# Optimization experiments

Hardware: AMD Instinct MI355X
Metric: run time of the kernel (lower is better)

## Reference

```python
import jax, jax.numpy as jnp
import numpy as np
import math

B, L, H, D = 4, 2048, 8, 64
FACTOR = 5
SAMPLE_K = min(FACTOR * int(np.ceil(np.log(L))), L)  # U_part = 40
N_TOP = min(FACTOR * int(np.ceil(np.log(L))), L)     # u = 40


def setup_inputs() -> dict:
    key = jax.random.key(0)
    kq, kk, kv, ki = jax.random.split(key, 4)
    queries = jax.random.normal(kq, (B, L, H, D), dtype=jnp.float32)
    keys = jax.random.normal(kk, (B, L, H, D), dtype=jnp.float32)
    values = jax.random.normal(kv, (B, L, H, D), dtype=jnp.float32)
    # ProbSparse random key sampling indices (torch.randint(L_K, (L_Q, sample_k)))
    index_sample = jax.random.randint(ki, (L, SAMPLE_K), 0, L, dtype=jnp.int64)
    return {"queries": queries, "keys": keys, "values": values,
            "index_sample": index_sample}


def reference(queries, keys, values, index_sample):
    # [B, L, H, D] -> [B, H, L, D]
    Q = jnp.transpose(queries, (0, 2, 1, 3))
    K = jnp.transpose(keys, (0, 2, 1, 3))
    V = jnp.transpose(values, (0, 2, 1, 3))
    L_K = K.shape[2]

    # --- _prob_QK ---
    # gather sampled keys per query: [B, H, L_Q, sample_k, D]
    K_sample = K[:, :, index_sample, :]
    # sampled QK dots: [B, H, L_Q, sample_k]
    Q_K_sample = jnp.einsum('bhld,bhlsd->bhls', Q, K_sample)
    # sparsity measurement M = max - mean
    M = Q_K_sample.max(axis=-1) - Q_K_sample.sum(axis=-1) / L_K  # [B, H, L_Q]
    _, M_top = jax.lax.top_k(M, N_TOP)  # [B, H, n_top]
    # gather top queries: [B, H, n_top, D]
    Q_reduce = jnp.take_along_axis(Q, M_top[..., None], axis=2)
    # reduced scores against all keys: [B, H, n_top, L_K]
    scores_top = jnp.einsum('bhud,bhkd->bhuk', Q_reduce, K)

    # --- forward tail ---
    scale = 1.0 / math.sqrt(D)
    attn = jax.nn.softmax(scores_top * scale, axis=-1)  # dropout = identity (eval)
    context = jnp.einsum('bhuk,bhkd->bhud', attn, V)  # [B, H, n_top, D]
    # [B, n_top, H, D]
    return jnp.transpose(context, (0, 2, 1, 3))
```

## Files before the change

### kernel.cpp

```cpp
#include <hip/hip_runtime.h>
#include <hip/hip_bf16.h>

#define BB 4
#define LL 2048
#define HH 8
#define DD 64
#define SK 40
#define NT 40
#define CH 256
#define NCH (LL / CH)
#define QH 20

#define WS 10
#define HB 68
#define RS (HH * HB)

__global__ __launch_bounds__(256) void compute_m_kernel(
        const float* __restrict__ Q, const float* __restrict__ K,
        const int* __restrict__ idx, float* __restrict__ M) {
    __shared__ float kbuf[4][2][2 * RS];
    __shared__ int sidx[SK];
    __shared__ float2 mlpart[4][HH];

    int blk = blockIdx.x;
    int x = blk & 7, g = blk >> 3;
    int b = x >> 1;
    int l = (g << 1) | (x & 1);
    int t = threadIdx.x;

    if (t < SK) sidx[t] = idx[(size_t)l * SK + t];

    int lane = t & 63, w = t >> 6;
    int s_lo = lane >> 5;
    int h    = (lane >> 2) & 7;
    int q    = lane & 3;

    const float4* Qb = (const float4*)(Q + ((size_t)b * LL + l) * 512 + h * 64 + q * 16);
    float4 qf0 = Qb[0], qf1 = Qb[1], qf2 = Qb[2], qf3 = Qb[3];

    const float* Kb = K + (size_t)b * LL * 512;

    int r  = lane >> 5;
    int cw = lane & 31;
    int av = cw >> 4;
    int c4 = (4 * cw) & 63;
    __syncthreads();

    float4 ra0, ra1, ra2, ra3;
    float4 rb0, rb1, rb2, rb3;

    #define LOADX(p, d0, d1, d2, d3) do {                                       \
        const float* src = Kb + (size_t)sidx[w * WS + (p) * 2 + r] * 512        \
                         + cw * 4;                                              \
        d0 = *(const float4*)(src);                                             \
        d1 = *(const float4*)(src + 128);                                       \
        d2 = *(const float4*)(src + 256);                                       \
        d3 = *(const float4*)(src + 384);                                       \
    } while (0)
    #define WRITEX(slot, d0, d1, d2, d3) do {                                   \
        float* base = &kbuf[w][slot][r * RS + c4];                              \
        *(float4*)(base + (av + 0) * HB) = d0;                                  \
        *(float4*)(base + (av + 2) * HB) = d1;                                  \
        *(float4*)(base + (av + 4) * HB) = d2;                                  \
        *(float4*)(base + (av + 6) * HB) = d3;                                  \
    } while (0)
    #define CONSUME(slot) do {                                                  \
        asm volatile("s_waitcnt lgkmcnt(0)" ::: "memory");                      \
        const float* kb = &kbuf[w][slot][s_lo * RS + h * HB + q * 16];          \
        float4 k0 = *(const float4*)(kb);                                       \
        float4 k1 = *(const float4*)(kb + 4);                                   \
        float4 k2 = *(const float4*)(kb + 8);                                   \
        float4 k3 = *(const float4*)(kb + 12);                                  \
        float pd = qf0.x*k0.x + qf0.y*k0.y + qf0.z*k0.z + qf0.w*k0.w            \
                 + qf1.x*k1.x + qf1.y*k1.y + qf1.z*k1.z + qf1.w*k1.w            \
                 + qf2.x*k2.x + qf2.y*k2.y + qf2.z*k2.z + qf2.w*k2.w            \
                 + qf3.x*k3.x + qf3.y*k3.y + qf3.z*k3.z + qf3.w*k3.w;           \
        pd += __shfl_xor(pd, 1, 64);                                            \
        pd += __shfl_xor(pd, 2, 64);                                            \
        mx = fmaxf(mx, pd);                                                     \
        sm += pd;                                                               \
    } while (0)

    float mx = -INFINITY, sm = 0.0f;

    LOADX(0, ra0, ra1, ra2, ra3);
    LOADX(1, rb0, rb1, rb2, rb3);
    WRITEX(0, ra0, ra1, ra2, ra3);

    LOADX(2, ra0, ra1, ra2, ra3);
    CONSUME(0);
    WRITEX(1, rb0, rb1, rb2, rb3);

    LOADX(3, rb0, rb1, rb2, rb3);
    CONSUME(1);
    WRITEX(0, ra0, ra1, ra2, ra3);

    LOADX(4, ra0, ra1, ra2, ra3);
    CONSUME(0);
    WRITEX(1, rb0, rb1, rb2, rb3);

    CONSUME(1);
    WRITEX(0, ra0, ra1, ra2, ra3);

    CONSUME(0);

    #undef LOADX
    #undef WRITEX
    #undef CONSUME

    mx = fmaxf(mx, __shfl_xor(mx, 32, 64));
    sm += __shfl_xor(sm, 32, 64);

    if ((lane & 0x23) == 0)
        mlpart[w][h] = make_float2(mx, sm);
    __syncthreads();

    if (t < HH) {
        float MX = -INFINITY, SM = 0.0f;
        #pragma unroll
        for (int w2 = 0; w2 < 4; ++w2) {
            float2 ml = mlpart[w2][t];
            MX = fmaxf(MX, ml.x);
            SM += ml.y;
        }
        M[((size_t)b * HH + t) * LL + l] = MX - SM * (1.0f / (float)LL);
    }
}

__global__ __launch_bounds__(256) void topk_kernel(const float* __restrict__ M,
                                                   int* __restrict__ topi) {
    __shared__ unsigned long long keys[LL];
    __shared__ unsigned long long wmax[4];
    __shared__ int win;
    int bh = blockIdx.x;
    int t  = threadIdx.x;
    int lane = t & 63, w = t >> 6;

    unsigned long long kmax = 0ULL;
    #pragma unroll
    for (int j = 0; j < 8; ++j) {
        int i = t + 256 * j;
        unsigned int bits = __float_as_uint(M[(size_t)bh * LL + i]);
        bits = (bits & 0x80000000u) ? ~bits : (bits | 0x80000000u);
        unsigned long long k = ((unsigned long long)bits << 11)
                             | (unsigned int)(LL - 1 - i);
        keys[i] = k;
        if (k > kmax) kmax = k;
    }
    __syncthreads();

    for (int u = 0; u < NT; ++u) {
        unsigned long long k = kmax;
        #pragma unroll
        for (int off = 32; off >= 1; off >>= 1) {
            unsigned long long o = __shfl_xor(k, off, 64);
            if (o > k) k = o;
        }
        if (lane == 0) wmax[w] = k;
        __syncthreads();
        if (t == 0) {
            unsigned long long k0 = wmax[0];
            if (wmax[1] > k0) k0 = wmax[1];
            if (wmax[2] > k0) k0 = wmax[2];
            if (wmax[3] > k0) k0 = wmax[3];
            int i = (LL - 1) - (int)(k0 & 0x7FF);
            topi[bh * NT + u] = i;
            keys[i] = 0ULL;
            win = i;
        }
        __syncthreads();
        if ((win & 255) == t) {
            kmax = 0ULL;
            #pragma unroll
            for (int j = 0; j < 8; ++j) {
                unsigned long long kk = keys[t + 256 * j];
                if (kk > kmax) kmax = kk;
            }
        }
    }
}

__global__ __launch_bounds__(256, 3) void attn_kernel(
        const float* __restrict__ Q, const float* __restrict__ K,
        const float* __restrict__ V, const int* __restrict__ topi,
        float2* __restrict__ pml, float* __restrict__ po) {
    __shared__ float  qs[QH][DD];
    __shared__ float4 e4buf[4][64];
    __shared__ float  oarea[4][QH][DD];
    __shared__ float  mlarea[4][QH][2];

    int blk = blockIdx.x;
    int qh  = blk >> 8;
    int cc2 = blk & 255;
    int c   = cc2 & (NCH - 1);
    int bh  = cc2 >> 3;
    int h = bh & (HH - 1), b = bh >> 3;
    int t = threadIdx.x, lane = t & 63, w = t >> 6;
    int u0 = qh * QH;

    for (int i = t; i < QH * DD; i += 256) {
        int u = i >> 6, d = i & 63;
        int lq = topi[bh * NT + u0 + u];
        qs[u][d] = Q[(((size_t)b * LL + lq) * HH + h) * DD + d];
    }

    int key = c * CH + w * 64 + lane;
    const float4* kr = (const float4*)&K[(((size_t)b * LL + key) * HH + h) * DD];
    float4 kreg[16];
    #pragma unroll
    for (int j = 0; j < 16; ++j) kreg[j] = kr[j];

    float vcol[64];
    const float* vb = &V[(((size_t)b * LL + c * CH + w * 64) * HH + h) * DD + lane];
    #pragma unroll
    for (int j = 0; j < 64; ++j) vcol[j] = vb[(size_t)j * HH * DD];

    __syncthreads();

    for (int uq = 0; uq < QH / 4; ++uq) {
        float o0 = 0, o1 = 0, o2 = 0, o3 = 0;
        float mv0, mv1, mv2, mv3, lv0, lv1, lv2, lv3;
        float4 ev;
        #pragma unroll
        for (int j = 0; j < 4; ++j) {
            int u = uq * 4 + j;
            const float4* q4 = (const float4*)&qs[u][0];
            float s = 0.0f;
            #pragma unroll
            for (int cc = 0; cc < 16; ++cc) {
                float4 qv = q4[cc];
                s += qv.x * kreg[cc].x + qv.y * kreg[cc].y
                   + qv.z * kreg[cc].z + qv.w * kreg[cc].w;
            }
            s *= 0.125f;
            float m = s;
            #pragma unroll
            for (int off = 32; off >= 1; off >>= 1)
                m = fmaxf(m, __shfl_xor(m, off, 64));
            float e = __expf(s - m);
            float ls = e;
            #pragma unroll
            for (int off = 32; off >= 1; off >>= 1)
                ls += __shfl_xor(ls, off, 64);
            if (j == 0) { mv0 = m; lv0 = ls; ev.x = e; }
            if (j == 1) { mv1 = m; lv1 = ls; ev.y = e; }
            if (j == 2) { mv2 = m; lv2 = ls; ev.z = e; }
            if (j == 3) { mv3 = m; lv3 = ls; ev.w = e; }
        }
        e4buf[w][lane] = ev;
        asm volatile("s_waitcnt lgkmcnt(0)" ::: "memory");
        #pragma unroll
        for (int l2 = 0; l2 < 64; ++l2) {
            float4 e = e4buf[w][l2];
            float  v = vcol[l2];
            o0 += e.x * v; o1 += e.y * v; o2 += e.z * v; o3 += e.w * v;
        }
        oarea[w][uq * 4 + 0][lane] = o0;
        oarea[w][uq * 4 + 1][lane] = o1;
        oarea[w][uq * 4 + 2][lane] = o2;
        oarea[w][uq * 4 + 3][lane] = o3;
        if (lane == 0) {
            mlarea[w][uq * 4 + 0][0] = mv0; mlarea[w][uq * 4 + 0][1] = lv0;
            mlarea[w][uq * 4 + 1][0] = mv1; mlarea[w][uq * 4 + 1][1] = lv1;
            mlarea[w][uq * 4 + 2][0] = mv2; mlarea[w][uq * 4 + 2][1] = lv2;
            mlarea[w][uq * 4 + 3][0] = mv3; mlarea[w][uq * 4 + 3][1] = lv3;
        }
    }
    __syncthreads();

    for (int i = t; i < QH * DD; i += 256) {
        int u = i >> 6, d = i & 63;
        float m0 = mlarea[0][u][0], m1 = mlarea[1][u][0];
        float m2 = mlarea[2][u][0], m3 = mlarea[3][u][0];
        float mb = fmaxf(fmaxf(m0, m1), fmaxf(m2, m3));
        float s0 = __expf(m0 - mb), s1 = __expf(m1 - mb);
        float s2 = __expf(m2 - mb), s3 = __expf(m3 - mb);
        float ob = oarea[0][u][d] * s0 + oarea[1][u][d] * s1
                 + oarea[2][u][d] * s2 + oarea[3][u][d] * s3;
        int gu = u0 + u;
        po[((size_t)(bh * NT + gu) * NCH + c) * DD + d] = ob;
        if (d == 0) {
            float lb = mlarea[0][u][1] * s0 + mlarea[1][u][1] * s1
                     + mlarea[2][u][1] * s2 + mlarea[3][u][1] * s3;
            pml[(bh * NT + gu) * NCH + c] = make_float2(mb, lb);
        }
    }
}

__global__ __launch_bounds__(256) void merge_kernel(
        const float2* __restrict__ pml, const float* __restrict__ po,
        float* __restrict__ out) {
    int wid  = blockIdx.x * 4 + (threadIdx.x >> 6);
    int lane = threadIdx.x & 63;
    int u  = wid % NT;
    int bh = wid / NT;
    int h = bh & (HH - 1), b = bh >> 3;
    int base = (bh * NT + u) * NCH;

    float m = -INFINITY;
    #pragma unroll
    for (int cc = 0; cc < NCH; ++cc) m = fmaxf(m, pml[base + cc].x);
    float lsum = 0.0f, o = 0.0f;
    #pragma unroll
    for (int cc = 0; cc < NCH; ++cc) {
        float2 ml = pml[base + cc];
        float sc = __expf(ml.x - m);
        lsum += ml.y * sc;
        o    += po[(size_t)(base + cc) * DD + lane] * sc;
    }
    out[(((size_t)b * NT + u) * HH + h) * DD + lane] = o / lsum;
}

extern "C" void kernel_launch(void* const* d_in, const int* in_sizes, int n_in,
                              void* d_out, int out_size, void* d_ws, size_t ws_size,
                              hipStream_t stream) {
    const float* Q   = (const float*)d_in[0];
    const float* K   = (const float*)d_in[1];
    const float* V   = (const float*)d_in[2];
    const int*   idx = (const int*)d_in[3];
    float* out = (float*)d_out;

    char* ws = (char*)d_ws;
    float*  M    = (float*)ws;                        ws += (size_t)BB * HH * LL * sizeof(float);
    int*    topi = (int*)ws;                          ws += (size_t)BB * HH * NT * sizeof(int);
    float2* pml  = (float2*)ws;                       ws += (size_t)BB * HH * NT * NCH * sizeof(float2);
    float*  po   = (float*)ws;

    hipLaunchKernelGGL(compute_m_kernel, dim3(BB * LL), dim3(256), 0, stream,
                       Q, K, idx, M);
    hipLaunchKernelGGL(topk_kernel, dim3(BB * HH), dim3(256), 0, stream, M, topi);
    hipLaunchKernelGGL(attn_kernel, dim3(2 * BB * HH * NCH), dim3(256), 0, stream,
                       Q, K, V, topi, pml, po);
    hipLaunchKernelGGL(merge_kernel, dim3(BB * HH * NT / 4), dim3(256), 0, stream,
                       pml, po, out);
}
```

Measured before the change: 167.9 us.

## Rewrite top-k as per-wave register selection and fuse merge via last-block atomic

The top-k kernel now keeps each wave's keys in registers and picks 40 candidates per wave with shuffle reductions and no block barriers inside the loop, then one wave does a final 40-of-160 selection. This removes the two __syncthreads per iteration and the shared-memory rescans. The separate merge kernel is removed: each attention block bumps a per-(b,h) atomic counter and the last block to finish does the cross-chunk softmax merge. That saves a launch but adds threadfences and leaves the merge tail to a single block per head.

```diff
diff --git a/kernel.cpp b/kernel.cpp
--- a/kernel.cpp
+++ b/kernel.cpp
@@ -128,54 +128,64 @@
 }
 
 __global__ __launch_bounds__(256) void topk_kernel(const float* __restrict__ M,
-                                                   int* __restrict__ topi) {
-    __shared__ unsigned long long keys[LL];
-    __shared__ unsigned long long wmax[4];
-    __shared__ int win;
+                                                   int* __restrict__ topi,
+                                                   int* __restrict__ cnt) {
+    __shared__ unsigned long long cand[4 * NT];
     int bh = blockIdx.x;
     int t  = threadIdx.x;
     int lane = t & 63, w = t >> 6;
 
+    if (t == 0) cnt[bh] = 0;
+
+    const float* Mb = M + (size_t)bh * LL + (w << 9);
+    unsigned long long k[8];
     unsigned long long kmax = 0ULL;
     #pragma unroll
     for (int j = 0; j < 8; ++j) {
-        int i = t + 256 * j;
-        unsigned int bits = __float_as_uint(M[(size_t)bh * LL + i]);
+        int i = (w << 9) + (j << 6) + lane;
+        unsigned int bits = __float_as_uint(Mb[(j << 6) + lane]);
         bits = (bits & 0x80000000u) ? ~bits : (bits | 0x80000000u);
-        unsigned long long k = ((unsigned long long)bits << 11)
-                             | (unsigned int)(LL - 1 - i);
-        keys[i] = k;
-        if (k > kmax) kmax = k;
-    }
-    __syncthreads();
-
+        k[j] = ((unsigned long long)bits << 11) | (unsigned int)(LL - 1 - i);
+        if (k[j] > kmax) kmax = k[j];
+    }
+
+    #pragma unroll 1
     for (int u = 0; u < NT; ++u) {
-        unsigned long long k = kmax;
+        unsigned long long m = kmax;
         #pragma unroll
         for (int off = 32; off >= 1; off >>= 1) {
-            unsigned long long o = __shfl_xor(k, off, 64);
-            if (o > k) k = o;
-        }
-        if (lane == 0) wmax[w] = k;
-        __syncthreads();
-        if (t == 0) {
-            unsigned long long k0 = wmax[0];
-            if (wmax[1] > k0) k0 = wmax[1];
-            if (wmax[2] > k0) k0 = wmax[2];
-            if (wmax[3] > k0) k0 = wmax[3];
-            int i = (LL - 1) - (int)(k0 & 0x7FF);
-            topi[bh * NT + u] = i;
-            keys[i] = 0ULL;
-            win = i;
-        }
-        __syncthreads();
-        if ((win & 255) == t) {
+            unsigned long long o = __shfl_xor(m, off, 64);
+            if (o > m) m = o;
+        }
+        if (lane == 0) cand[w * NT + u] = m;
+        if (kmax == m) {
+            #pragma unroll
+            for (int j = 0; j < 8; ++j) if (k[j] == m) k[j] = 0ULL;
             kmax = 0ULL;
             #pragma unroll
-            for (int j = 0; j < 8; ++j) {
-                unsigned long long kk = keys[t + 256 * j];
-                if (kk > kmax) kmax = kk;
+            for (int j = 0; j < 8; ++j) if (k[j] > kmax) kmax = k[j];
+        }
+    }
+    __syncthreads();
+
+    if (w == 0) {
+        unsigned long long a0 = cand[lane];
+        unsigned long long a1 = cand[lane + 64];
+        unsigned long long a2 = (lane + 128 < 4 * NT) ? cand[lane + 128] : 0ULL;
+        #pragma unroll 1
+        for (int u = 0; u < NT; ++u) {
+            unsigned long long m = a0;
+            if (a1 > m) m = a1;
+            if (a2 > m) m = a2;
+            #pragma unroll
+            for (int off = 32; off >= 1; off >>= 1) {
+                unsigned long long o = __shfl_xor(m, off, 64);
+                if (o > m) m = o;
             }
+            if (lane == 0) topi[bh * NT + u] = (LL - 1) - (int)(m & 0x7FF);
+            if (a0 == m) a0 = 0ULL;
+            if (a1 == m) a1 = 0ULL;
+            if (a2 == m) a2 = 0ULL;
         }
     }
 }
@@ -183,11 +193,12 @@
 __global__ __launch_bounds__(256, 3) void attn_kernel(
         const float* __restrict__ Q, const float* __restrict__ K,
         const float* __restrict__ V, const int* __restrict__ topi,
-        float2* __restrict__ pml, float* __restrict__ po) {
+        float2* pml, float* po, int* cnt, float* __restrict__ out) {
     __shared__ float  qs[QH][DD];
     __shared__ float4 e4buf[4][64];
     __shared__ float  oarea[4][QH][DD];
     __shared__ float  mlarea[4][QH][2];
+    __shared__ int    amlast;
 
     int blk = blockIdx.x;
     int qh  = blk >> 8;
@@ -285,30 +296,32 @@
             pml[(bh * NT + gu) * NCH + c] = make_float2(mb, lb);
         }
     }
-}
-
-__global__ __launch_bounds__(256) void merge_kernel(
-        const float2* __restrict__ pml, const float* __restrict__ po,
-        float* __restrict__ out) {
-    int wid  = blockIdx.x * 4 + (threadIdx.x >> 6);
-    int lane = threadIdx.x & 63;
-    int u  = wid % NT;
-    int bh = wid / NT;
-    int h = bh & (HH - 1), b = bh >> 3;
-    int base = (bh * NT + u) * NCH;
-
-    float m = -INFINITY;
-    #pragma unroll
-    for (int cc = 0; cc < NCH; ++cc) m = fmaxf(m, pml[base + cc].x);
-    float lsum = 0.0f, o = 0.0f;
-    #pragma unroll
-    for (int cc = 0; cc < NCH; ++cc) {
-        float2 ml = pml[base + cc];
-        float sc = __expf(ml.x - m);
-        lsum += ml.y * sc;
-        o    += po[(size_t)(base + cc) * DD + lane] * sc;
-    }
-    out[(((size_t)b * NT + u) * HH + h) * DD + lane] = o / lsum;
+
+    __threadfence();
+    if (t == 0) {
+        int old = atomicAdd(&cnt[bh], 1);
+        amlast = (old == 2 * NCH - 1);
+    }
+    __syncthreads();
+    if (amlast) {
+        __threadfence();
+        for (int i = t; i < NT * DD; i += 256) {
+            int u = i >> 6, d = i & 63;
+            int base = (bh * NT + u) * NCH;
+            float m = -INFINITY;
+            #pragma unroll
+            for (int cc = 0; cc < NCH; ++cc) m = fmaxf(m, pml[base + cc].x);
+            float lsum = 0.0f, o = 0.0f;
+            #pragma unroll
+            for (int cc = 0; cc < NCH; ++cc) {
+                float2 ml = pml[base + cc];
+                float sc = __expf(ml.x - m);
+                lsum += ml.y * sc;
+                o    += po[(size_t)(base + cc) * DD + d] * sc;
+            }
+            out[(((size_t)b * NT + u) * HH + h) * DD + d] = o / lsum;
+        }
+    }
 }
 
 extern "C" void kernel_launch(void* const* d_in, const int* in_sizes, int n_in,
@@ -324,13 +337,12 @@
     float*  M    = (float*)ws;                        ws += (size_t)BB * HH * LL * sizeof(float);
     int*    topi = (int*)ws;                          ws += (size_t)BB * HH * NT * sizeof(int);
     float2* pml  = (float2*)ws;                       ws += (size_t)BB * HH * NT * NCH * sizeof(float2);
-    float*  po   = (float*)ws;
+    float*  po   = (float*)ws;                        ws += (size_t)BB * HH * NT * NCH * DD * sizeof(float);
+    int*    cnt  = (int*)ws;
 
     hipLaunchKernelGGL(compute_m_kernel, dim3(BB * LL), dim3(256), 0, stream,
                        Q, K, idx, M);
-    hipLaunchKernelGGL(topk_kernel, dim3(BB * HH), dim3(256), 0, stream, M, topi);
+    hipLaunchKernelGGL(topk_kernel, dim3(BB * HH), dim3(256), 0, stream, M, topi, cnt);
     hipLaunchKernelGGL(attn_kernel, dim3(2 * BB * HH * NCH), dim3(256), 0, stream,
-                       Q, K, V, topi, pml, po);
-    hipLaunchKernelGGL(merge_kernel, dim3(BB * HH * NT / 4), dim3(256), 0, stream,
-                       pml, po, out);
+                       Q, K, V, topi, pml, po, cnt, out);
 }
```

New measurement: 226.5 us. 34.9% more time.
